# Optimization experiments

Hardware: AMD Instinct MI355X
Metric: run time of the kernel (lower is better)

The kernel has to match this reference:

```python
import jax, jax.numpy as jnp
import numpy as np
from jax import lax

B, N, D = 4, 64, 32  # graphs, nodes/graph, volume side
HC = 1024            # hidden_channels
NF = 2048            # num_node_features = 32*(D//8)**3
NC = 4               # num_classes
LC = 256             # linear_channels = N*(HC//4)//64


def setup_inputs() -> dict:
    key = jax.random.key(0)
    ks = jax.random.split(key, 16)
    x = jax.random.normal(ks[0], (B, N, D, D, D), jnp.float32)
    # binary symmetric adjacency, zero diagonal (edge presence only; GCNConv ignores values)
    u = jax.random.uniform(ks[1], (B, N, N))
    a = (u < 0.2).astype(jnp.int32)
    a = jnp.maximum(a, a.transpose(0, 2, 1)) * (1 - jnp.eye(N, dtype=jnp.int32))
    s = 0.05
    inp = dict(
        x=x, adj=a, batch_size=B,
        w_conv1=jax.random.normal(ks[2], (16, 1, 3, 3, 3), jnp.float32) * s,
        b_conv1=jnp.zeros((16,), jnp.float32),
        w_conv2=jax.random.normal(ks[3], (32, 16, 3, 3, 3), jnp.float32) * s,
        b_conv2=jnp.zeros((32,), jnp.float32),
        w_g1=jax.random.normal(ks[4], (NF, HC), jnp.float32) * s,
        b_g1=jnp.zeros((HC,), jnp.float32),
        w_g2=jax.random.normal(ks[5], (HC, HC // 2), jnp.float32) * s,
        b_g2=jnp.zeros((HC // 2,), jnp.float32),
        w_g3=jax.random.normal(ks[6], (HC // 2, HC // 4), jnp.float32) * s,
        b_g3=jnp.zeros((HC // 4,), jnp.float32),
        w_fc1=jax.random.normal(ks[7], (LC, 2 * LC), jnp.float32) * s,
        b_fc1=jnp.zeros((2 * LC,), jnp.float32),
        w_fc2=jax.random.normal(ks[8], (2 * LC, NC), jnp.float32) * s,
        b_fc2=jnp.zeros((NC,), jnp.float32),
    )
    return inp


DN = ('NCDHW', 'OIDHW', 'NCDHW')


def _maxpool3(h):
    # MaxPool3d(kernel=3, stride=2, padding=1); pad value -inf matches torch
    return lax.reduce_window(h, -jnp.inf, lax.max,
                             (1, 1, 3, 3, 3), (1, 1, 2, 2, 2),
                             [(0, 0), (0, 0), (1, 1), (1, 1), (1, 1)])


def _gcn_norm(adj, dtype):
    # GCNConv: A_hat = A + I, sym-normalized D^-1/2 A_hat D^-1/2 (per graph)
    A = (adj != 0).astype(dtype) + jnp.eye(adj.shape[-1], dtype=dtype)[None]
    deg = A.sum(-1)                        # [B, N], >= 1
    dinv = deg ** -0.5
    return A * dinv[:, :, None] * dinv[:, None, :]


def _forward(x, adj, batch_size, w_conv1, b_conv1, w_conv2, b_conv2,
             w_g1, b_g1, w_g2, b_g2, w_g3, b_g3, w_fc1, b_fc1, w_fc2, b_fc2):
    b, n = x.shape[0], x.shape[1]
    v = x.reshape(b * n, 1, x.shape[2], x.shape[3], x.shape[4])
    h = lax.conv_general_dilated(v, w_conv1, (1, 1, 1), [(1, 1)] * 3, dimension_numbers=DN)
    h = jax.nn.relu(h + b_conv1[None, :, None, None, None])
    h = _maxpool3(h)                                     # [BN,16,16,16,16]
    h = lax.conv_general_dilated(h, w_conv2, (2, 2, 2), [(1, 1)] * 3, dimension_numbers=DN)
    h = jax.nn.relu(h + b_conv2[None, :, None, None, None])
    h = _maxpool3(h)                                     # [BN,32,4,4,4]
    feat = h.reshape(b, n, -1)                           # [B,N,2048]

    A_norm = _gcn_norm(adj, feat.dtype)                  # [B,N,N]
    gcn = lambda X, W, bb: jnp.einsum('bij,bjf->bif', A_norm, X @ W) + bb
    g = jax.nn.relu(gcn(feat, w_g1, b_g1))
    g = jax.nn.relu(gcn(g, w_g2, b_g2))
    g = gcn(g, w_g3, b_g3)                               # [B,N,256] (no relu, matches source)

    g = g.reshape(batch_size, -1)                        # [B, 16384]
    g = g.reshape(batch_size, -1, 64).max(-1)            # MaxPool1d(64) on 2D input -> [B,256]
    g = jax.nn.relu(g @ w_fc1 + b_fc1)
    return jax.nn.softmax(g @ w_fc2 + b_fc2, axis=-1)


def reference(x, adj, batch_size, w_conv1, b_conv1, w_conv2, b_conv2,
              w_g1, b_g1, w_g2, b_g2, w_g3, b_g3, w_fc1, b_fc1, w_fc2, b_fc2):
    return _forward(x, adj, batch_size, w_conv1, b_conv1, w_conv2, b_conv2,
                    w_g1, b_g1, w_g2, b_g2, w_g3, b_g3, w_fc1, b_fc1, w_fc2, b_fc2)
```

## Files before the change

### kernel.cpp

```cpp
#include <hip/hip_runtime.h>

typedef unsigned short ushort_t;
typedef __attribute__((ext_vector_type(8))) short bf16x8;
typedef __attribute__((ext_vector_type(4))) float f32x4;

static __device__ __forceinline__ unsigned short f2bf(float f) {
  unsigned u = __float_as_uint(f);
  u = (u + 0x7FFFu + ((u >> 16) & 1u)) >> 16;
  return (unsigned short)u;
}

static __device__ __forceinline__ f32x4 max4(f32x4 a, f32x4 b) {
  f32x4 r;
  r[0] = fmaxf(a[0], b[0]); r[1] = fmaxf(a[1], b[1]);
  r[2] = fmaxf(a[2], b[2]); r[3] = fmaxf(a[3], b[3]);
  return r;
}


__device__ __forceinline__ void prep_transpose(
    const float* __restrict__ W, ushort_t* __restrict__ out,
    int K, int N, int n0, int k0, int t, float (*tile)[33])
{
  const int tx = t & 31, ty = t >> 5;
#pragma unroll
  for (int i = 0; i < 4; ++i) {
    const int k = k0 + ty + i * 8;
    tile[ty + i * 8][tx] = W[(size_t)k * N + n0 + tx];
  }
  __syncthreads();
#pragma unroll
  for (int i = 0; i < 4; ++i) {
    const int n = n0 + ty + i * 8;
    out[(size_t)n * K + k0 + tx] = f2bf(tile[tx][ty + i * 8]);
  }
}

__global__ __launch_bounds__(256) void k_prep(
    const float* __restrict__ x, ushort_t* __restrict__ xb16,
    const float* __restrict__ w2, ushort_t* __restrict__ w2f,
    const float* __restrict__ wg1, ushort_t* __restrict__ wg1T,
    const float* __restrict__ wg2, ushort_t* __restrict__ wg2T,
    const float* __restrict__ wg3, ushort_t* __restrict__ wg3T,
    const int* __restrict__ adj, float* __restrict__ An)
{
  __shared__ float tile[32][33];
  __shared__ float dinv[64];
  __shared__ int part[256];
  int b = blockIdx.x;
  const int t = threadIdx.x;
  if (b < 8192) {
    const int tid = b * 256 + t;
    const float4 v = ((const float4*)x)[tid];
    const unsigned lo = (unsigned)f2bf(v.x) | ((unsigned)f2bf(v.y) << 16);
    const unsigned hi = (unsigned)f2bf(v.z) | ((unsigned)f2bf(v.w) << 16);
    ((uint2*)xb16)[tid] = make_uint2(lo, hi);
    return;
  }
  b -= 8192;
  if (b < 56) {
    const int tid = b * 256 + t;
    if (tid < 14336) {
      const int nt = tid / 7168, rem = tid % 7168;
      const int kk = rem / 512, rem2 = rem % 512;
      const int l = rem2 >> 3, j = rem2 & 7;
      const int n = nt * 16 + (l & 15);
      const int k = (l >> 4) * 8 + kk * 32 + j;
      float v = 0.f;
      if (k < 432) v = w2[n * 432 + k];
      w2f[tid] = f2bf(v);
    }
    return;
  }
  b -= 56;
  if (b < 2048) { prep_transpose(wg1, wg1T, 2048, 1024, (b & 31) << 5, (b >> 5) << 5, t, tile); return; }
  b -= 2048;
  if (b < 512)  { prep_transpose(wg2, wg2T, 1024, 512,  (b & 15) << 5, (b >> 4) << 5, t, tile); return; }
  b -= 512;
  if (b < 128)  { prep_transpose(wg3, wg3T, 512,  256,  (b & 7)  << 5, (b >> 3) << 5, t, tile); return; }
  b -= 128;
  {
    const int i = t >> 2, q = t & 3;
    const int* ab = adj + b * 4096 + i * 64 + q * 16;
    int d = 0;
#pragma unroll
    for (int j = 0; j < 16; ++j) d += (ab[j] != 0) ? 1 : 0;
    part[t] = d;
    __syncthreads();
    if (q == 0)
      dinv[i] = rsqrtf((float)(1 + part[t] + part[t + 1] + part[t + 2] + part[t + 3]));
    __syncthreads();
    for (int idx = t; idx < 4096; idx += 256) {
      const int ii = idx >> 6, jj = idx & 63;
      const float a = (ii == jj) ? 1.f : ((adj[b * 4096 + idx] != 0) ? 1.f : 0.f);
      An[b * 4096 + idx] = a * dinv[ii] * dinv[jj];
    }
  }
}

__global__ __launch_bounds__(256) void k_conv1_mfma(
    const ushort_t* __restrict__ xb16, const float* __restrict__ wc,
    const float* __restrict__ bc, ushort_t* __restrict__ h1)
{
  __shared__ ushort_t L[2 * 34 * 76];
  char* Lb = (char*)L;
  const int bn = blockIdx.x >> 3, zg = blockIdx.x & 7;
  const int t = threadIdx.x;
  const int w = t >> 6, l = t & 63;
  const int grp = l >> 4, m = l & 15, ch = l & 15;
  const float NINF = -1e30f;

  union { short s[8]; bf16x8 v; } uA, uB;
#pragma unroll
  for (int j = 0; j < 8; ++j) {
    const int k = grp * 8 + j;
    float wA = 0.f, wB = 0.f;
    if (k < 12) {
      const int dx = k >> 2, dz = k & 3;
      if (dz < 3) { wA = wc[ch*27 + dz*9 + 0 + dx]; wB = wc[ch*27 + dz*9 + 6 + dx]; }
    } else if (k >= 16 && k < 28) {
      const int kk = k - 16, dx = kk >> 2, dz = kk & 3;
      if (dz < 3) wA = wc[ch*27 + dz*9 + 3 + dx];
    }
    uA.s[j] = (short)f2bf(wA);
    uB.s[j] = (short)f2bf(wB);
  }

  int aX1[3], aX2[3];
#pragma unroll
  for (int s = 0; s < 3; ++s) {
    const int Q1 = 2*m + s + 2*(grp & 1);
    const int Q2 = Q1 + 1;
    aX1[s] = (Q1 & 1) * 5168 + (Q1 >> 1) * 8;
    aX2[s] = (Q2 & 1) * 5168 + (Q2 >> 1) * 8;
  }
  const int rsel = (grp >> 1) * 152;

  for (int u = t; u < 200; u += 256) {
    int addr;
    if (u < 72) {
      const int rr = (u < 36) ? 0 : 33;
      const int s = (u < 36) ? u : u - 36;
      const int pp = s / 18, slot = s - pp * 18;
      addr = pp * 5168 + rr * 152 + slot * 8;
    } else {
      const int v = u - 72;
      const int rr = 1 + (v >> 2);
      const int pp = (v >> 1) & 1;
      const int slot = (v & 1) * 17;
      addr = pp * 5168 + rr * 152 + slot * 8;
    }
    *(unsigned long long*)(Lb + addr) = 0ull;
  }

  f32x4 accZ[4][2];
#pragma unroll
  for (int j = 0; j < 4; ++j)
#pragma unroll
    for (int p = 0; p < 2; ++p) accZ[j][p] = (f32x4){NINF, NINF, NINF, NINF};

  const ushort_t* xb = xb16 + (size_t)bn * 32768;

#pragma unroll 1
  for (int ci = 0; ci < 5; ++ci) {
    const int cz = 4*zg - 1 + ci;
    if (cz < 0) continue;
    if (t < 128) {
      const int r = 1 + (t >> 2), g = t & 3;
      const ushort_t* xrow = xb + (r - 1) * 32 + g * 8;
      uint4 u0 = make_uint4(0u, 0u, 0u, 0u), u2 = make_uint4(0u, 0u, 0u, 0u);
      if (cz > 0)  u0 = *(const uint4*)(xrow + (cz - 1) * 1024);
      const uint4 u1 = *(const uint4*)(xrow + cz * 1024);
      if (cz < 31) u2 = *(const uint4*)(xrow + (cz + 1) * 1024);
      char* b0 = Lb + r * 152 + (4 * g + 1) * 8;
      char* b1 = Lb + 5168 + r * 152 + (4 * g + 1) * 8;
      const unsigned* p0 = (const unsigned*)&u0;
      const unsigned* p1 = (const unsigned*)&u1;
      const unsigned* p2 = (const unsigned*)&u2;
#pragma unroll
      for (int e = 0; e < 4; ++e) {
        const unsigned w0 = p0[e], w1 = p1[e], w2v = p2[e];
        const unsigned lo_e = (w0 & 0xFFFFu) | (w1 << 16);
        const unsigned hi_e = (w2v & 0xFFFFu);
        const unsigned lo_o = (w0 >> 16) | (w1 & 0xFFFF0000u);
        const unsigned hi_o = (w2v >> 16);
        *(unsigned long long*)(b0 + e * 8) =
            (unsigned long long)lo_e | ((unsigned long long)hi_e << 32);
        *(unsigned long long*)(b1 + e * 8) =
            (unsigned long long)lo_o | ((unsigned long long)hi_o << 32);
      }
    }
    __syncthreads();
    f32x4 accP0 = (f32x4){NINF, NINF, NINF, NINF};
    f32x4 accP1 = (f32x4){NINF, NINF, NINF, NINF};
#pragma unroll
    for (int yy = 0; yy < 9; ++yy) {
      if (yy == 0 && w == 0) continue;
      const int y = 8 * w - 1 + yy;
      const int rbA = y * 152 + rsel;
      const int rbB = (y + 2) * 152;
      f32x4 Cy;
#pragma unroll
      for (int s = 0; s < 3; ++s) {
        union { unsigned long long u[2]; bf16x8 v; } fA, fB;
        fA.u[0] = *(const unsigned long long*)(Lb + aX1[s] + rbA);
        fA.u[1] = *(const unsigned long long*)(Lb + aX2[s] + rbA);
        fB.u[0] = *(const unsigned long long*)(Lb + aX1[s] + rbB);
        fB.u[1] = *(const unsigned long long*)(Lb + aX2[s] + rbB);
        f32x4 acc = (f32x4){0.f, 0.f, 0.f, 0.f};
        acc = __builtin_amdgcn_mfma_f32_16x16x32_bf16(fA.v, uA.v, acc, 0, 0, 0);
        acc = __builtin_amdgcn_mfma_f32_16x16x32_bf16(fB.v, uB.v, acc, 0, 0, 0);
        if (s == 0) acc[0] = (l < 16) ? NINF : acc[0];
        Cy = (s == 0) ? acc : max4(Cy, acc);
      }
      if (yy & 1) {
        const int c = (yy - 1) / 2;
        if ((c & 1) == 0) accP0 = max4(accP0, Cy); else accP1 = max4(accP1, Cy);
      } else {
        const int cl = yy / 2 - 1;
        const int chh = yy / 2;
        if (cl >= 0) {
          if ((cl & 1) == 0) {
            accP0 = max4(accP0, Cy);
            if (ci <= 2) accZ[cl][0] = max4(accZ[cl][0], accP0);
            if (ci >= 2) accZ[cl][1] = max4(accZ[cl][1], accP0);
            accP0 = (f32x4){NINF, NINF, NINF, NINF};
          } else {
            accP1 = max4(accP1, Cy);
            if (ci <= 2) accZ[cl][0] = max4(accZ[cl][0], accP1);
            if (ci >= 2) accZ[cl][1] = max4(accZ[cl][1], accP1);
            accP1 = (f32x4){NINF, NINF, NINF, NINF};
          }
        }
        if (chh <= 3) {
          if ((chh & 1) == 0) accP0 = max4(accP0, Cy); else accP1 = max4(accP1, Cy);
        }
      }
    }
    __syncthreads();
  }

  const float biasv = bc[ch];
#pragma unroll
  for (int j = 0; j < 4; ++j) {
    const int py = 4 * w + j;
#pragma unroll
    for (int p = 0; p < 2; ++p) {
      const int pz = 2 * zg + p;
      const f32x4 v = accZ[j][p];
      const unsigned lo = (unsigned)f2bf(fmaxf(v[0] + biasv, 0.f)) |
                          ((unsigned)f2bf(fmaxf(v[1] + biasv, 0.f)) << 16);
      const unsigned hi = (unsigned)f2bf(fmaxf(v[2] + biasv, 0.f)) |
                          ((unsigned)f2bf(fmaxf(v[3] + biasv, 0.f)) << 16);
      ushort_t* dst = h1 + (((size_t)(bn * 16 + ch) * 16 + pz) << 8) + py * 16 + grp * 4;
      *(uint2*)dst = make_uint2(lo, hi);
    }
  }
}

__global__ __launch_bounds__(128) void k_conv2(
    const ushort_t* __restrict__ h1, const ushort_t* __restrict__ w2f,
    float* __restrict__ c2)
{
  __shared__ ushort_t As[16 * 456];
  const int b = blockIdx.x;
  const int bn = b >> 5, oz = (b >> 2) & 7, yg = b & 3;
  const int t = threadIdx.x;
  const ushort_t* hb = h1 + ((size_t)bn << 16);
  const int w = t >> 6, l = t & 63;

  bf16x8 bfr[14];
#pragma unroll
  for (int kk = 0; kk < 14; ++kk)
    bfr[kk] = *(const bf16x8*)(const void*)&w2f[(((w * 14) + kk) * 64 + l) * 8];

  for (int idx = t; idx < 256; idx += 128) {
    const int r = idx >> 4, k = 432 + (idx & 15);
    As[r * 456 + k] = 0;
  }

  const int m = t >> 3, sub = t & 7;
  const int oy = 2 * yg + (m >> 3), ox = m & 7;
  ushort_t tv[54];
  int j = 0;
#pragma unroll
  for (int ic2 = 0; ic2 < 2; ++ic2) {
    const ushort_t* icp = hb + ((sub * 2 + ic2) << 12);
#pragma unroll
    for (int dz = 0; dz < 3; ++dz) {
      const int iz = 2 * oz - 1 + dz;
      const bool zok = (unsigned)iz < 16u;
      const unsigned* zp = (const unsigned*)(icp + (iz << 8));
#pragma unroll
      for (int dy = 0; dy < 3; ++dy) {
        const int iy = 2 * oy - 1 + dy;
        const bool yok = zok && ((unsigned)iy < 16u);
        const unsigned* ydw = zp + (iy << 3);
        const unsigned d0 = (yok && ox > 0) ? ydw[ox - 1] : 0u;
        const unsigned d1 = yok ? ydw[ox] : 0u;
        tv[j]     = (ushort_t)(d0 >> 16);
        tv[j + 1] = (ushort_t)(d1 & 0xFFFFu);
        tv[j + 2] = (ushort_t)(d1 >> 16);
        j += 3;
      }
    }
  }
  {
    unsigned* Aw = (unsigned*)As;
    const int wbase = m * 228 + sub * 27;
#pragma unroll
    for (int p = 0; p < 27; ++p)
      Aw[wbase + p] = (unsigned)tv[2 * p] | ((unsigned)tv[2 * p + 1] << 16);
  }
  __syncthreads();
  f32x4 acc = {0.f, 0.f, 0.f, 0.f};
  const ushort_t* arow = &As[(l & 15) * 456 + ((l >> 4) << 3)];
#pragma unroll
  for (int kk = 0; kk < 14; ++kk) {
    const bf16x8 af = *(const bf16x8*)(const void*)&arow[kk * 32];
    acc = __builtin_amdgcn_mfma_f32_16x16x32_bf16(af, bfr[kk], acc, 0, 0, 0);
  }
  const int n = w * 16 + (l & 15);
  const int m0 = (l >> 4) << 2;
  float* cb = c2 + (((size_t)(bn * 32 + n) * 8) + oz) * 64 + yg * 16 + m0;
  *(float4*)cb = make_float4(acc[0], acc[1], acc[2], acc[3]);
}

__global__ __launch_bounds__(256) void k_pool2(
    const float* __restrict__ c2, const float* __restrict__ bc2,
    ushort_t* __restrict__ featb)
{
  const int tid = blockIdx.x * 256 + threadIdx.x;
  const int bn = tid >> 9, r = tid & 511;
  const int ch = r >> 4, pz = (r >> 2) & 3, py = r & 3;
  const float* base = c2 + ((size_t)(bn * 32 + ch) << 9);
  float m0 = -1e30f, m1 = -1e30f, m2 = -1e30f, m3 = -1e30f;
#pragma unroll
  for (int dz = 0; dz < 3; ++dz) {
    const int oz = 2 * pz - 1 + dz;
    if ((unsigned)oz >= 8u) continue;
#pragma unroll
    for (int dy = 0; dy < 3; ++dy) {
      const int oy = 2 * py - 1 + dy;
      if ((unsigned)oy >= 8u) continue;
      const float* row = base + (oz << 6) + (oy << 3);
      const float4 a = ((const float4*)row)[0];
      const float4 b = ((const float4*)row)[1];
      m0 = fmaxf(m0, fmaxf(a.x, a.y));
      m1 = fmaxf(m1, fmaxf(a.y, fmaxf(a.z, a.w)));
      m2 = fmaxf(m2, fmaxf(a.w, fmaxf(b.x, b.y)));
      m3 = fmaxf(m3, fmaxf(b.y, fmaxf(b.z, b.w)));
    }
  }
  const float bb = bc2[ch];
  const unsigned lo = (unsigned)f2bf(fmaxf(m0 + bb, 0.f)) |
                      ((unsigned)f2bf(fmaxf(m1 + bb, 0.f)) << 16);
  const unsigned hi = (unsigned)f2bf(fmaxf(m2 + bb, 0.f)) |
                      ((unsigned)f2bf(fmaxf(m3 + bb, 0.f)) << 16);
  *(uint2*)(featb + (size_t)bn * 2048 + r * 4) = make_uint2(lo, hi);
}

__global__ __launch_bounds__(256) void k_gcn_layer(
    const ushort_t* __restrict__ Xb, const ushort_t* __restrict__ WT,
    const float* __restrict__ bias, const float* __restrict__ An,
    ushort_t* __restrict__ Ob, float* __restrict__ Of, int K, int N, int relu)
{
  __shared__ ushort_t As[64 * 72];
  __shared__ ushort_t Bs[64 * 72];
  __shared__ ushort_t Ps[64 * 72];
  const int b = blockIdx.y, jb = blockIdx.x << 6;
  const int t = threadIdx.x, w = t >> 6, l = t & 63;
  const int r0 = t >> 3, kc0 = t & 7;
  const int lm = l & 15, lg = l >> 4;

  union { short s[8]; bf16x8 v; } afr[2];
  {
    const float* ap = An + b * 4096 + (16 * w + lm) * 64 + (lg << 3);
#pragma unroll
    for (int kc = 0; kc < 2; ++kc) {
      const float4 v0 = *(const float4*)(ap + kc * 32);
      const float4 v1 = *(const float4*)(ap + kc * 32 + 4);
      afr[kc].s[0] = (short)f2bf(v0.x); afr[kc].s[1] = (short)f2bf(v0.y);
      afr[kc].s[2] = (short)f2bf(v0.z); afr[kc].s[3] = (short)f2bf(v0.w);
      afr[kc].s[4] = (short)f2bf(v1.x); afr[kc].s[5] = (short)f2bf(v1.y);
      afr[kc].s[6] = (short)f2bf(v1.z); afr[kc].s[7] = (short)f2bf(v1.w);
    }
  }

  f32x4 acc[4];
#pragma unroll
  for (int nt = 0; nt < 4; ++nt) acc[nt] = (f32x4){0.f, 0.f, 0.f, 0.f};

#pragma unroll 1
  for (int kt = 0; kt < K; kt += 64) {
    __syncthreads();
#pragma unroll
    for (int h = 0; h < 2; ++h) {
      const int row = r0 + h * 32;
      const uint4 va = *(const uint4*)&Xb[(size_t)(b * 64 + row) * K + kt + kc0 * 8];
      *(uint4*)&As[row * 72 + kc0 * 8] = va;
      const uint4 vb = *(const uint4*)&WT[(size_t)(jb + row) * K + kt + kc0 * 8];
      *(uint4*)&Bs[row * 72 + kc0 * 8] = vb;
    }
    __syncthreads();
#pragma unroll
    for (int ks = 0; ks < 2; ++ks) {
      const bf16x8 af = *(const bf16x8*)(const void*)
          &As[(16 * w + lm) * 72 + ks * 32 + (lg << 3)];
#pragma unroll
      for (int nt = 0; nt < 4; ++nt) {
        const bf16x8 bf = *(const bf16x8*)(const void*)
            &Bs[(nt * 16 + lm) * 72 + ks * 32 + (lg << 3)];
        acc[nt] = __builtin_amdgcn_mfma_f32_16x16x32_bf16(af, bf, acc[nt], 0, 0, 0);
      }
    }
  }

  const int m0 = lg << 2;
#pragma unroll
  for (int nt = 0; nt < 4; ++nt) {
    const int n = nt * 16 + lm;
    const unsigned lo = (unsigned)f2bf(acc[nt][0]) | ((unsigned)f2bf(acc[nt][1]) << 16);
    const unsigned hi = (unsigned)f2bf(acc[nt][2]) | ((unsigned)f2bf(acc[nt][3]) << 16);
    *(uint2*)&Ps[n * 72 + 16 * w + m0] = make_uint2(lo, hi);
  }
  __syncthreads();

#pragma unroll
  for (int nt = 0; nt < 4; ++nt) {
    const bf16x8 b0 = *(const bf16x8*)(const void*)&Ps[(nt * 16 + lm) * 72 + (lg << 3)];
    const bf16x8 b1 = *(const bf16x8*)(const void*)&Ps[(nt * 16 + lm) * 72 + 32 + (lg << 3)];
    f32x4 a2 = (f32x4){0.f, 0.f, 0.f, 0.f};
    a2 = __builtin_amdgcn_mfma_f32_16x16x32_bf16(afr[0].v, b0, a2, 0, 0, 0);
    a2 = __builtin_amdgcn_mfma_f32_16x16x32_bf16(afr[1].v, b1, a2, 0, 0, 0);
    const int col = jb + nt * 16 + lm;
    const float bv = bias[col];
#pragma unroll
    for (int r = 0; r < 4; ++r) {
      const int row = b * 64 + 16 * w + m0 + r;
      float v = a2[r] + bv;
      if (relu) v = fmaxf(v, 0.f);
      if (Ob) Ob[(size_t)row * N + col] = f2bf(v);
      else    Of[(size_t)row * N + col] = v;
    }
  }
}

__global__ __launch_bounds__(256) void k_head(
    const float* __restrict__ g3, const float* __restrict__ w1, const float* __restrict__ b1,
    const float* __restrict__ w2, const float* __restrict__ b2, float* __restrict__ out)
{
  const int b = blockIdx.x, t = threadIdx.x;
  __shared__ float sp[256];
  __shared__ float sh[512];
  __shared__ float sl[4];
  {
    const int n = t >> 2, c = t & 3;
    const float* gr = g3 + (size_t)(b * 64 + n) * 256 + c * 64;
    float mx = -1e30f;
    for (int f = 0; f < 64; ++f) mx = fmaxf(mx, gr[f]);
    sp[t] = mx;
  }
  __syncthreads();
  for (int jj = t; jj < 512; jj += 256) {
    float s = b1[jj];
    for (int k = 0; k < 256; ++k) s += sp[k] * w1[k * 512 + jj];
    sh[jj] = fmaxf(s, 0.f);
  }
  __syncthreads();
  if (t < 4) {
    float s = b2[t];
    for (int k = 0; k < 512; ++k) s += sh[k] * w2[k * 4 + t];
    sl[t] = s;
  }
  __syncthreads();
  if (t == 0) {
    const float mm = fmaxf(fmaxf(sl[0], sl[1]), fmaxf(sl[2], sl[3]));
    const float e0 = expf(sl[0] - mm), e1 = expf(sl[1] - mm);
    const float e2 = expf(sl[2] - mm), e3 = expf(sl[3] - mm);
    const float inv = 1.f / (e0 + e1 + e2 + e3);
    out[b * 4 + 0] = e0 * inv;
    out[b * 4 + 1] = e1 * inv;
    out[b * 4 + 2] = e2 * inv;
    out[b * 4 + 3] = e3 * inv;
  }
}

extern "C" void kernel_launch(void* const* d_in, const int* in_sizes, int n_in,
                              void* d_out, int out_size, void* d_ws, size_t ws_size,
                              hipStream_t stream)
{
  (void)in_sizes; (void)n_in; (void)out_size; (void)ws_size;
  const float* x   = (const float*)d_in[0];
  const int*   adj = (const int*)d_in[1];
  const float* wc1 = (const float*)d_in[3];
  const float* bc1 = (const float*)d_in[4];
  const float* wc2 = (const float*)d_in[5];
  const float* bc2 = (const float*)d_in[6];
  const float* wg1 = (const float*)d_in[7];
  const float* bg1 = (const float*)d_in[8];
  const float* wg2 = (const float*)d_in[9];
  const float* bg2 = (const float*)d_in[10];
  const float* wg3 = (const float*)d_in[11];
  const float* bg3 = (const float*)d_in[12];
  const float* wf1 = (const float*)d_in[13];
  const float* bf1 = (const float*)d_in[14];
  const float* wf2 = (const float*)d_in[15];
  const float* bf2 = (const float*)d_in[16];

  float* ws    = (float*)d_ws;
  ushort_t* h1 = (ushort_t*)d_ws;
  ushort_t* w2f   = (ushort_t*)(ws + 8388608);
  ushort_t* wg1Tb = (ushort_t*)(ws + 8395776);
  ushort_t* wg2Tb = (ushort_t*)(ws + 9444352);
  ushort_t* wg3Tb = (ushort_t*)(ws + 9706496);
  ushort_t* featb = (ushort_t*)(ws + 9772032);
  ushort_t* g1b   = (ushort_t*)(ws + 10034176);
  ushort_t* g2b   = (ushort_t*)(ws + 10165248);
  float* c2    = ws + 16777216;
  ushort_t* xb16 = (ushort_t*)(ws + 16777216);
  float* An   = ws + 21495808;
  float* g3   = ws + 22364160;
  float* outp = (float*)d_out;

  hipLaunchKernelGGL(k_prep,        dim3(10940),    dim3(256), 0, stream,
                     x, xb16, wc2, w2f, wg1, wg1Tb, wg2, wg2Tb, wg3, wg3Tb, adj, An);
  hipLaunchKernelGGL(k_conv1_mfma,  dim3(2048),     dim3(256), 0, stream, xb16, wc1, bc1, h1);
  hipLaunchKernelGGL(k_conv2,       dim3(8192),     dim3(128), 0, stream, h1, w2f, c2);
  hipLaunchKernelGGL(k_pool2,       dim3(512),      dim3(256), 0, stream, c2, bc2, featb);
  hipLaunchKernelGGL(k_gcn_layer,   dim3(16,4),     dim3(256), 0, stream,
                     featb, wg1Tb, bg1, An, g1b, (float*)nullptr, 2048, 1024, 1);
  hipLaunchKernelGGL(k_gcn_layer,   dim3(8,4),      dim3(256), 0, stream,
                     g1b, wg2Tb, bg2, An, g2b, (float*)nullptr, 1024, 512, 1);
  hipLaunchKernelGGL(k_gcn_layer,   dim3(4,4),      dim3(256), 0, stream,
                     g2b, wg3Tb, bg3, An, (ushort_t*)nullptr, g3, 512, 256, 0);
  hipLaunchKernelGGL(k_head,        dim3(4),        dim3(256), 0, stream, g3, wf1, bf1, wf2, bf2, outp);
}
```

Baseline: 288.7 us.

## Double-buffer GCN layer tiles with register prefetch; precompute conv1 LDS addresses

The GCN layer GEMM now uses two LDS buffers for the A and B tiles. It prefetches the next K-slice from global memory into registers while MFMAs run on the current buffer, which removes one barrier per iteration. This is meant to hide global load latency in a kernel with only a few blocks. The conv1 kernel now precomputes per-lane LDS base pointers so the inner loop needs only a constant row offset, cutting address arithmetic. LDS use in the GCN kernel grows, and register pressure rises from the held prefetch values.

```diff
diff --git a/kernel.cpp b/kernel.cpp
--- a/kernel.cpp
+++ b/kernel.cpp
@@ -1,6 +1,7 @@
 #include <hip/hip_runtime.h>
 
 typedef unsigned short ushort_t;
+typedef unsigned long long ull_t;
 typedef __attribute__((ext_vector_type(8))) short bf16x8;
 typedef __attribute__((ext_vector_type(4))) float f32x4;
 
@@ -126,15 +127,24 @@
     uB.s[j] = (short)f2bf(wB);
   }
 
-  int aX1[3], aX2[3];
-#pragma unroll
-  for (int s = 0; s < 3; ++s) {
-    const int Q1 = 2*m + s + 2*(grp & 1);
-    const int Q2 = Q1 + 1;
-    aX1[s] = (Q1 & 1) * 5168 + (Q1 >> 1) * 8;
-    aX2[s] = (Q2 & 1) * 5168 + (Q2 >> 1) * 8;
-  }
-  const int rsel = (grp >> 1) * 152;
+  const char* baseA[3][2];
+  const char* baseB[3][2];
+  {
+    const int rsel = (grp >> 1) * 152;
+    const int rowA = (8 * w - 1) * 152 + rsel;
+    const int rowB = (8 * w + 1) * 152;
+#pragma unroll
+    for (int s = 0; s < 3; ++s) {
+      const int Q1 = 2*m + s + 2*(grp & 1);
+      const int Q2 = Q1 + 1;
+      const int aX1 = (Q1 & 1) * 5168 + (Q1 >> 1) * 8;
+      const int aX2 = (Q2 & 1) * 5168 + (Q2 >> 1) * 8;
+      baseA[s][0] = Lb + (aX1 + rowA);
+      baseA[s][1] = Lb + (aX2 + rowA);
+      baseB[s][0] = Lb + (aX1 + rowB);
+      baseB[s][1] = Lb + (aX2 + rowB);
+    }
+  }
 
   for (int u = t; u < 200; u += 256) {
     int addr;
@@ -150,7 +160,7 @@
       const int slot = (v & 1) * 17;
       addr = pp * 5168 + rr * 152 + slot * 8;
     }
-    *(unsigned long long*)(Lb + addr) = 0ull;
+    *(ull_t*)(Lb + addr) = 0ull;
   }
 
   f32x4 accZ[4][2];
@@ -184,10 +194,8 @@
         const unsigned hi_e = (w2v & 0xFFFFu);
         const unsigned lo_o = (w0 >> 16) | (w1 & 0xFFFF0000u);
         const unsigned hi_o = (w2v >> 16);
-        *(unsigned long long*)(b0 + e * 8) =
-            (unsigned long long)lo_e | ((unsigned long long)hi_e << 32);
-        *(unsigned long long*)(b1 + e * 8) =
-            (unsigned long long)lo_o | ((unsigned long long)hi_o << 32);
+        *(ull_t*)(b0 + e * 8) = (ull_t)lo_e | ((ull_t)hi_e << 32);
+        *(ull_t*)(b1 + e * 8) = (ull_t)lo_o | ((ull_t)hi_o << 32);
       }
     }
     __syncthreads();
@@ -196,17 +204,14 @@
 #pragma unroll
     for (int yy = 0; yy < 9; ++yy) {
       if (yy == 0 && w == 0) continue;
-      const int y = 8 * w - 1 + yy;
-      const int rbA = y * 152 + rsel;
-      const int rbB = (y + 2) * 152;
       f32x4 Cy;
 #pragma unroll
       for (int s = 0; s < 3; ++s) {
-        union { unsigned long long u[2]; bf16x8 v; } fA, fB;
-        fA.u[0] = *(const unsigned long long*)(Lb + aX1[s] + rbA);
-        fA.u[1] = *(const unsigned long long*)(Lb + aX2[s] + rbA);
-        fB.u[0] = *(const unsigned long long*)(Lb + aX1[s] + rbB);
-        fB.u[1] = *(const unsigned long long*)(Lb + aX2[s] + rbB);
+        union { ull_t u[2]; bf16x8 v; } fA, fB;
+        fA.u[0] = *(const ull_t*)(baseA[s][0] + yy * 152);
+        fA.u[1] = *(const ull_t*)(baseA[s][1] + yy * 152);
+        fB.u[0] = *(const ull_t*)(baseB[s][0] + yy * 152);
+        fB.u[1] = *(const ull_t*)(baseB[s][1] + yy * 152);
         f32x4 acc = (f32x4){0.f, 0.f, 0.f, 0.f};
         acc = __builtin_amdgcn_mfma_f32_16x16x32_bf16(fA.v, uA.v, acc, 0, 0, 0);
         acc = __builtin_amdgcn_mfma_f32_16x16x32_bf16(fB.v, uB.v, acc, 0, 0, 0);
@@ -241,6 +246,7 @@
   }
 
   const float biasv = bc[ch];
+  const int grp4 = grp * 4;
 #pragma unroll
   for (int j = 0; j < 4; ++j) {
     const int py = 4 * w + j;
@@ -252,7 +258,7 @@
                           ((unsigned)f2bf(fmaxf(v[1] + biasv, 0.f)) << 16);
       const unsigned hi = (unsigned)f2bf(fmaxf(v[2] + biasv, 0.f)) |
                           ((unsigned)f2bf(fmaxf(v[3] + biasv, 0.f)) << 16);
-      ushort_t* dst = h1 + (((size_t)(bn * 16 + ch) * 16 + pz) << 8) + py * 16 + grp * 4;
+      ushort_t* dst = h1 + (((size_t)(bn * 16 + ch) * 16 + pz) << 8) + py * 16 + grp4;
       *(uint2*)dst = make_uint2(lo, hi);
     }
   }
@@ -365,8 +371,8 @@
     const float* __restrict__ bias, const float* __restrict__ An,
     ushort_t* __restrict__ Ob, float* __restrict__ Of, int K, int N, int relu)
 {
-  __shared__ ushort_t As[64 * 72];
-  __shared__ ushort_t Bs[64 * 72];
+  __shared__ ushort_t As[2][64 * 72];
+  __shared__ ushort_t Bs[2][64 * 72];
   __shared__ ushort_t Ps[64 * 72];
   const int b = blockIdx.y, jb = blockIdx.x << 6;
   const int t = threadIdx.x, w = t >> 6, l = t & 63;
@@ -391,31 +397,45 @@
 #pragma unroll
   for (int nt = 0; nt < 4; ++nt) acc[nt] = (f32x4){0.f, 0.f, 0.f, 0.f};
 
+  const ushort_t* arow0 = &Xb[(size_t)(b * 64 + r0) * K + kc0 * 8];
+  const ushort_t* arow1 = &Xb[(size_t)(b * 64 + r0 + 32) * K + kc0 * 8];
+  const ushort_t* brow0 = &WT[(size_t)(jb + r0) * K + kc0 * 8];
+  const ushort_t* brow1 = &WT[(size_t)(jb + r0 + 32) * K + kc0 * 8];
+
+  uint4 va0 = *(const uint4*)arow0;
+  uint4 va1 = *(const uint4*)arow1;
+  uint4 vb0 = *(const uint4*)brow0;
+  uint4 vb1 = *(const uint4*)brow1;
+
+  int buf = 0;
 #pragma unroll 1
   for (int kt = 0; kt < K; kt += 64) {
+    *(uint4*)&As[buf][r0 * 72 + kc0 * 8]        = va0;
+    *(uint4*)&As[buf][(r0 + 32) * 72 + kc0 * 8] = va1;
+    *(uint4*)&Bs[buf][r0 * 72 + kc0 * 8]        = vb0;
+    *(uint4*)&Bs[buf][(r0 + 32) * 72 + kc0 * 8] = vb1;
     __syncthreads();
-#pragma unroll
-    for (int h = 0; h < 2; ++h) {
-      const int row = r0 + h * 32;
-      const uint4 va = *(const uint4*)&Xb[(size_t)(b * 64 + row) * K + kt + kc0 * 8];
-      *(uint4*)&As[row * 72 + kc0 * 8] = va;
-      const uint4 vb = *(const uint4*)&WT[(size_t)(jb + row) * K + kt + kc0 * 8];
-      *(uint4*)&Bs[row * 72 + kc0 * 8] = vb;
-    }
-    __syncthreads();
+    if (kt + 64 < K) {
+      va0 = *(const uint4*)(arow0 + kt + 64);
+      va1 = *(const uint4*)(arow1 + kt + 64);
+      vb0 = *(const uint4*)(brow0 + kt + 64);
+      vb1 = *(const uint4*)(brow1 + kt + 64);
+    }
 #pragma unroll
     for (int ks = 0; ks < 2; ++ks) {
       const bf16x8 af = *(const bf16x8*)(const void*)
-          &As[(16 * w + lm) * 72 + ks * 32 + (lg << 3)];
+          &As[buf][(16 * w + lm) * 72 + ks * 32 + (lg << 3)];
 #pragma unroll
       for (int nt = 0; nt < 4; ++nt) {
         const bf16x8 bf = *(const bf16x8*)(const void*)
-            &Bs[(nt * 16 + lm) * 72 + ks * 32 + (lg << 3)];
+            &Bs[buf][(nt * 16 + lm) * 72 + ks * 32 + (lg << 3)];
         acc[nt] = __builtin_amdgcn_mfma_f32_16x16x32_bf16(af, bf, acc[nt], 0, 0, 0);
       }
     }
-  }
-
+    buf ^= 1;
+  }
+
+  __syncthreads();
   const int m0 = lg << 2;
 #pragma unroll
   for (int nt = 0; nt < 4; ++nt) {
```

Result: faster. 280.0 us (-3.0%).
